# Performance work log

Hardware: AMD Instinct MI355X
Metric: run time of the kernel (lower is better)

Reference implementation:

```python
import jax, jax.numpy as jnp
import numpy as np
from jax.scipy.linalg import cho_solve

N, D, K, M = 2048, 128, 8, 64
JITTER = 1e-5


def setup_inputs() -> dict:
    key = jax.random.key(0)
    ks = jax.random.split(key, 5)
    X = jax.random.normal(ks[0], (N, D), jnp.float32)
    Y = jax.random.normal(ks[1], (N, 1), jnp.float32)
    q_mu = 0.1 * jax.random.normal(ks[2], (K, D), jnp.float32)
    # positive variational covariances ~ 1/D, as in the original init
    q_cov = jax.random.uniform(ks[3], (K, D), jnp.float32, 0.5 / D, 1.5 / D)
    Z = jax.random.normal(ks[4], (M, K), jnp.float32)
    sigma_f = jnp.float32(1.0)
    noise_var = jnp.float32(0.01)
    return {"X": X, "Y": Y, "q_mu": q_mu, "q_cov": q_cov, "Z": Z,
            "sigma_f": sigma_f, "noise_var": noise_var}


def _compute_psi1(X, q_mu, q_cov, Z, sigma_f):
    # q_mu_X: (K, N)
    q_mu_X = jnp.einsum('kd,nd->kn', q_mu, X)
    # top: (K, N, M)
    top = (q_mu_X[:, :, None] - Z.T[:, None, :]) ** 2
    # bot: (K, N)
    bot = 1.0 + jnp.einsum('kd,nd->kn', q_cov, X * X)
    bot = bot[:, :, None]
    psi1 = jnp.exp(-0.5 * top / bot) / jnp.sqrt(bot)  # (K, N, M)
    return sigma_f * jnp.prod(psi1, axis=0)  # (N, M)


def _compute_batched_psi2(X, q_mu, q_cov, Z, sigma_f):
    q_mu_X = jnp.einsum('kd,nd->kn', q_mu, X)  # (K, N)
    Z_diff = Z[:, None, :] - Z[None, :, :]      # (M, M, K)
    Z_bar = 0.5 * (Z[:, None, :] + Z[None, :, :])  # (M, M, K)
    # top: (K, N, M, M) -- the dominant intermediate
    top = (q_mu_X[:, :, None, None] - jnp.transpose(Z_bar, (2, 0, 1))[:, None, :, :]) ** 2
    bot = 2.0 * jnp.einsum('kd,nd->kn', q_cov, X * X) + 1.0  # (K, N)
    bot = bot[:, :, None, None]
    right = jnp.prod(jnp.exp(-top / bot) / jnp.sqrt(bot), axis=0)  # (N, M, M)
    left = (sigma_f ** 2) * jnp.exp(-0.25 * jnp.sum(Z_diff ** 2, axis=2))  # (M, M)
    return left * right  # (N, M, M)


def _rbf_K(Z):
    # ARD RBF with unit variance and unit lengthscales (frozen in original)
    sq = jnp.sum((Z[:, None, :] - Z[None, :, :]) ** 2, axis=-1)
    return jnp.exp(-0.5 * sq)


def _chol_logdet(chol):
    return 2.0 * jnp.sum(jnp.log(jnp.diagonal(chol)), axis=-1)


def _elbo(X, Y, q_mu, q_cov, Z, sigma_f, noise_var):
    n = X.shape[0]
    d = X.shape[1]
    m = Z.shape[0]
    sigma2 = jnp.reshape(noise_var, ())
    sf = jnp.reshape(sigma_f, ())
    two_pi = jnp.asarray(2.0 * np.pi, X.dtype)
    eye = jnp.eye(m, dtype=X.dtype)

    Kuu = _rbf_K(Z) + eye * JITTER
    chol_Ku = jnp.linalg.cholesky(Kuu)
    F1 = -n * jnp.log(two_pi) - (n - m) * jnp.log(sigma2) + _chol_logdet(chol_Ku)

    YY = Y.T @ Y  # (1, 1)
    psi2 = jnp.sum(_compute_batched_psi2(X, q_mu, q_cov, Z, sf), axis=0)  # (M, M)
    Ku_Psi2 = sigma2 * Kuu + psi2 + eye * JITTER
    chol_Ku_Psi2 = jnp.linalg.cholesky(Ku_Psi2)
    F1 = F1 - _chol_logdet(chol_Ku_Psi2) - YY / sigma2  # (1, 1)

    psi1 = _compute_psi1(X, q_mu, q_cov, Z, sf)  # (N, M)
    Psi1_Y = psi1.T @ Y  # (M, 1)
    F1 = F1 + (Psi1_Y.T @ cho_solve((chol_Ku_Psi2, True), Psi1_Y)) / sigma2

    psi0 = n * sf ** 2
    KuiPsi2 = cho_solve((chol_Ku, True), psi2)
    F1 = F1 - psi0 / sigma2 + jnp.trace(KuiPsi2) / sigma2

    KL = jnp.sum(jnp.log(q_cov), axis=1)
    KL = KL - d * jnp.log(jnp.sum(q_cov + q_mu ** 2, axis=1))
    KL = KL + d * jnp.asarray(np.log(d), X.dtype)
    KL = jnp.sum(KL)
    return jnp.squeeze(0.5 * (F1 + KL))


def reference(X, Y, q_mu, q_cov, Z, sigma_f, noise_var):
    return _elbo(X, Y, q_mu, q_cov, Z, sigma_f, noise_var)
```

## Files before the change

kernel.cpp:

```cpp
#include <hip/hip_runtime.h>
#include <math.h>

namespace {
constexpr int N_ = 2048;
constexpr int D_ = 128;
constexpr int K_ = 8;
constexpr int M_ = 64;
constexpr float JIT = 1e-5f;
constexpr float L2E = 1.4426950408889634f;
constexpr float LN2 = 0.6931471805599453f;

constexpr int OFF_ARR2 = 32;
constexpr int OFF_C2   = OFF_ARR2 + N_ * 16;
constexpr int OFF_ARR1 = OFF_C2 + N_;
constexpr int OFF_CY   = OFF_ARR1 + N_ * 16;
constexpr int OFF_P2P  = OFF_CY + N_;
constexpr int OFF_P1Y  = OFF_P2P + 16 * 4096;
constexpr int OFF_PSI2 = OFF_P1Y + 512;
constexpr int OFF_KUI  = OFF_PSI2 + 4096;
constexpr int OFF_SC   = OFF_KUI + 4096;
}

struct F8 { float f[8]; };

__device__ __forceinline__ void bar_arrive(int* c) {
  __syncthreads();
  if (threadIdx.x == 0) { __threadfence(); atomicAdd(c, 1); }
}
template <int SLP>
__device__ __forceinline__ void bar_wait(int* c, int target) {
  if (threadIdx.x == 0) {
    while (__hip_atomic_load(c, __ATOMIC_RELAXED, __HIP_MEMORY_SCOPE_AGENT) < target)
      __builtin_amdgcn_s_sleep(SLP);
    __threadfence();
  }
  __syncthreads();
}

__device__ __forceinline__ float sweep2x2_pipe(
    float* reg, float (*rowbuf)[2][M_], int wave, int lane) {
  if (wave == 0) {
    rowbuf[0][0][lane] = reg[0];
    rowbuf[0][1][lane] = reg[1];
  }
  __syncthreads();
  float ld = 0.f;
#pragma unroll
  for (int s = 0; s < 32; ++s) {
    const int p = 2 * s;
    const int par = s & 1;
    float* rbA = rowbuf[par][0];
    float* rbB = rowbuf[par][1];
    const int own_s  = s >> 3;
    const int own_s1 = (s + 1) >> 3;
    const int rp  = p & 15;
    const int rp2 = (p + 2) & 15;

    const float P00 = rbA[p];
    const float P01 = rbA[p + 1];
    const float P11 = rbB[p + 1];
    const float a0  = rbA[lane];
    const float a1  = rbB[lane];
    const float det = fmaf(P00, P11, -P01 * P01);
    const float idet = __builtin_amdgcn_rcpf(det);
    ld += __log2f(det);
    const float Pi00 =  P11 * idet;
    const float Pi01 = -P01 * idet;
    const float Pi11 =  P00 * idet;

    const bool isp = (lane == p), isq = (lane == p + 1);
    const float w0 = isp ? Pi00 : (isq ? Pi01 : fmaf(Pi00, a0, Pi01 * a1));
    const float w1 = isp ? Pi01 : (isq ? Pi11 : fmaf(Pi01, a0, Pi11 * a1));
    const float t0 = isp ? (1.f - w0) : (isq ? -w0 : w0);
    const float t1 = isq ? (1.f - w1) : (isp ? -w1 : w1);
    const float f0 = (isp || isq) ? -w0 : w0;
    const float f1 = (isp || isq) ? -w1 : w1;

    if (s < 31 && wave == own_s1) {
      const float e0 = fmaf(-t1, rbB[p + 2], fmaf(-t0, rbA[p + 2], reg[rp2]));
      const float e1 = fmaf(-t1, rbB[p + 3], fmaf(-t0, rbA[p + 3], reg[rp2 + 1]));
      rowbuf[par ^ 1][0][lane] = e0;
      rowbuf[par ^ 1][1][lane] = e1;
    }

    const float4* rAq = reinterpret_cast<const float4*>(rbA + 16 * wave);
    const float4* rBq = reinterpret_cast<const float4*>(rbB + 16 * wave);
#pragma unroll
    for (int q = 0; q < 4; q++) {
      const float4 va = rAq[q], vb = rBq[q];
      reg[4 * q + 0] = fmaf(-t1, vb.x, fmaf(-t0, va.x, reg[4 * q + 0]));
      reg[4 * q + 1] = fmaf(-t1, vb.y, fmaf(-t0, va.y, reg[4 * q + 1]));
      reg[4 * q + 2] = fmaf(-t1, vb.z, fmaf(-t0, va.z, reg[4 * q + 2]));
      reg[4 * q + 3] = fmaf(-t1, vb.w, fmaf(-t0, va.w, reg[4 * q + 3]));
    }
    if (wave == own_s) { reg[rp] = f0; reg[rp + 1] = f1; }
    __syncthreads();
  }
  return ld;
}

__global__ __launch_bounds__(256) void vdmgp_k1(
    const float* __restrict__ X, const float* __restrict__ Y,
    const float* __restrict__ qmu, const float* __restrict__ qcov,
    const float* __restrict__ Z, float* __restrict__ ws) {
  __shared__ float smu[D_ * K_];
  __shared__ float scov[D_ * K_];
  __shared__ float zl[M_][9];
  __shared__ __align__(16) float rowbuf[2][2][M_];
  const int tid = threadIdx.x;
  const int b = blockIdx.x;

  if (b == 0 && tid < 32) ((int*)ws)[tid] = 0;

  if (b == 8) {
    for (int idx = tid; idx < M_ * K_; idx += 256) zl[idx >> 3][idx & 7] = Z[idx];
    __syncthreads();
    const int lane = tid & 63;
    const int wave = tid >> 6;
    float zj[K_];
#pragma unroll
    for (int k = 0; k < K_; k++) zj[k] = zl[lane][k];
    float reg[16];
#pragma unroll
    for (int r = 0; r < 16; r++) {
      const int gi = 16 * wave + r;
      float sq = 0.f;
#pragma unroll
      for (int k = 0; k < K_; k++) { const float dd = zl[gi][k] - zj[k]; sq = fmaf(dd, dd, sq); }
      reg[r] = exp2f(-0.5f * L2E * sq) + ((gi == lane) ? JIT : 0.f);
    }
    const float ld1 = sweep2x2_pipe(reg, rowbuf, wave, lane);
#pragma unroll
    for (int r = 0; r < 16; r++)
      ws[OFF_KUI + (16 * wave + r) * 64 + lane] = reg[r];
    if (tid == 0) ws[OFF_SC + 2] = LN2 * ld1;
    return;
  }

  if (b == 9) {
    const int lane = tid & 63;
    const int wave = tid >> 6;
    if (wave == 0) {
      float yy = 0.f;
#pragma unroll
      for (int t = 0; t < 32; t++) {
        const float y = Y[t * 64 + lane];
        yy = fmaf(y, y, yy);
      }
#pragma unroll
      for (int off = 32; off > 0; off >>= 1) yy += __shfl_down(yy, off, 64);
      if (lane == 0) ws[OFF_SC + 0] = yy;
    } else if (wave == 1) {
      const int k = lane >> 3;
      const int d0 = (lane & 7) * 16;
      float slog = 0.f, srow = 0.f;
#pragma unroll
      for (int t = 0; t < 16; t++) {
        const float qc = qcov[k * D_ + d0 + t];
        const float qm = qmu[k * D_ + d0 + t];
        slog += logf(qc);
        srow += qc + qm * qm;
      }
#pragma unroll
      for (int off = 4; off > 0; off >>= 1) {
        slog += __shfl_down(slog, off, 8);
        srow += __shfl_down(srow, off, 8);
      }
      float klr = ((lane & 7) == 0)
          ? (slog - (float)D_ * logf(srow) + (float)D_ * logf((float)D_)) : 0.f;
      klr += __shfl_down(klr, 32, 64);
      klr += __shfl_down(klr, 16, 64);
      klr += __shfl_down(klr, 8, 64);
      if (lane == 0) ws[OFF_SC + 1] = klr;
    }
    return;
  }

  for (int idx = tid; idx < K_ * D_; idx += 256) {
    int k = idx >> 7, d = idx & 127;
    smu[d * K_ + k]  = qmu[idx];
    scov[d * K_ + k] = qcov[idx];
  }
  __syncthreads();

  const int n = b * 256 + tid;
  float a[K_], s2[K_];
#pragma unroll
  for (int k = 0; k < K_; k++) { a[k] = 0.f; s2[k] = 0.f; }

  const float4* xrow = reinterpret_cast<const float4*>(X + n * D_);
#pragma unroll 2
  for (int dq = 0; dq < D_ / 4; dq++) {
    float4 xv = xrow[dq];
    float xs[4] = {xv.x, xv.y, xv.z, xv.w};
#pragma unroll
    for (int t = 0; t < 4; t++) {
      const int d = dq * 4 + t;
      const float x = xs[t];
      const float xx = x * x;
      F8 mu = *reinterpret_cast<const F8*>(&smu[d * K_]);
      F8 cv = *reinterpret_cast<const F8*>(&scov[d * K_]);
#pragma unroll
      for (int k = 0; k < K_; k++) {
        a[k]  = fmaf(mu.f[k], x, a[k]);
        s2[k] = fmaf(cv.f[k], xx, s2[k]);
      }
    }
  }

  float4 w2[4], w1[4];
  float prod2 = 1.f, prod1 = 1.f;
#pragma unroll
  for (int k = 0; k < K_; k++) {
    const float b2 = 2.f * s2[k] + 1.f;
    const float b1 = 1.f + s2[k];
    reinterpret_cast<float*>(w2)[k]     = a[k];
    reinterpret_cast<float*>(w2)[8 + k] = L2E / b2;
    reinterpret_cast<float*>(w1)[k]     = a[k];
    reinterpret_cast<float*>(w1)[8 + k] = 0.5f * L2E / b1;
    prod2 *= rsqrtf(b2);
    prod1 *= rsqrtf(b1);
  }
  float4* a2q = reinterpret_cast<float4*>(ws + OFF_ARR2 + n * 16);
  float4* a1q = reinterpret_cast<float4*>(ws + OFF_ARR1 + n * 16);
#pragma unroll
  for (int e = 0; e < 4; e++) { a2q[e] = w2[e]; a1q[e] = w1[e]; }
  (ws + OFF_C2)[n] = prod2;
  (ws + OFF_CY)[n] = prod1 * Y[n];
}

__global__ __launch_bounds__(256) void vdmgp_k2(
    const float* __restrict__ Z,
    const float* __restrict__ sfp, const float* __restrict__ nvp,
    float* __restrict__ ws, float* __restrict__ out) {
  __shared__ __align__(16) float pool[4864];

  int* bar = (int*)ws;
  const int tid = threadIdx.x;
  const int b = blockIdx.x;
  const float sf = sfp[0];

  if (b > 0) {
    const int t = b - 1;
    {
      float* sa = pool;
      float* sc = pool + 2048;
      const int chunk = t >> 4;
      const int nbase = chunk * 128;
      const float4* src = reinterpret_cast<const float4*>(ws + OFF_ARR2 + nbase * 16);
      float4* dst = reinterpret_cast<float4*>(sa);
      for (int idx = tid; idx < 128 * 4; idx += 256) dst[idx] = src[idx];
      if (tid < 128) sc[tid] = (ws + OFF_C2)[nbase + tid];
      __syncthreads();

      const int pair = (t & 15) * 256 + tid;
      const int i = pair >> 6, j = pair & 63;
      float zb[K_];
#pragma unroll
      for (int k = 0; k < K_; k++) zb[k] = 0.5f * (Z[i * K_ + k] + Z[j * K_ + k]);

      float acc = 0.f;
      for (int nl = 0; nl < 128; nl += 4) {
        F8 av0 = *reinterpret_cast<const F8*>(&sa[(nl + 0) * 16]);
        F8 ib0 = *reinterpret_cast<const F8*>(&sa[(nl + 0) * 16 + 8]);
        F8 av1 = *reinterpret_cast<const F8*>(&sa[(nl + 1) * 16]);
        F8 ib1 = *reinterpret_cast<const F8*>(&sa[(nl + 1) * 16 + 8]);
        F8 av2 = *reinterpret_cast<const F8*>(&sa[(nl + 2) * 16]);
        F8 ib2 = *reinterpret_cast<const F8*>(&sa[(nl + 2) * 16 + 8]);
        F8 av3 = *reinterpret_cast<const F8*>(&sa[(nl + 3) * 16]);
        F8 ib3 = *reinterpret_cast<const F8*>(&sa[(nl + 3) * 16 + 8]);
        float s0 = 0.f, s1 = 0.f, s2 = 0.f, s3 = 0.f;
#pragma unroll
        for (int k = 0; k < K_; k++) {
          const float d0 = av0.f[k] - zb[k]; s0 = fmaf(d0 * d0, ib0.f[k], s0);
          const float d1 = av1.f[k] - zb[k]; s1 = fmaf(d1 * d1, ib1.f[k], s1);
          const float d2 = av2.f[k] - zb[k]; s2 = fmaf(d2 * d2, ib2.f[k], s2);
          const float d3 = av3.f[k] - zb[k]; s3 = fmaf(d3 * d3, ib3.f[k], s3);
        }
        acc = fmaf(sc[nl + 0], exp2f(-s0), acc);
        acc = fmaf(sc[nl + 1], exp2f(-s1), acc);
        acc = fmaf(sc[nl + 2], exp2f(-s2), acc);
        acc = fmaf(sc[nl + 3], exp2f(-s3), acc);
      }
      (ws + OFF_P2P)[chunk * 4096 + (t & 15) * 256 + tid] = acc;
    }
    bar_arrive(&bar[t & 15]);

    if (t < 16) {
      bar_wait<4>(&bar[t], 16);
      const int p = t * 256 + tid;
      float acc = 0.f;
#pragma unroll
      for (int c = 0; c < 16; c++) acc += ws[OFF_P2P + c * 4096 + p];
      const int i = p >> 6, j = p & 63;
      float sq = 0.f;
#pragma unroll
      for (int k = 0; k < K_; k++) {
        const float dd = Z[i * K_ + k] - Z[j * K_ + k];
        sq = fmaf(dd, dd, sq);
      }
      ws[OFF_PSI2 + p] = sf * sf * exp2f(-0.25f * L2E * sq) * acc;
      bar_arrive(&bar[17]);
    } else if (t < 24) {
      float* sa1 = pool;
      float* scy = pool + 4096;
      float* red = pool + 4352;
      const int chunk = t - 16;
      const int nbase = chunk * 256;
      const float4* src = reinterpret_cast<const float4*>(ws + OFF_ARR1 + nbase * 16);
      float4* dst = reinterpret_cast<float4*>(sa1);
#pragma unroll
      for (int r = 0; r < 4; r++) dst[r * 256 + tid] = src[r * 256 + tid];
      scy[tid] = (ws + OFF_CY)[nbase + tid];
      __syncthreads();

      const int m = tid & 63;
      const int stripe = tid >> 6;
      float zm[K_];
#pragma unroll
      for (int k = 0; k < K_; k++) zm[k] = Z[m * K_ + k];

      float acc = 0.f;
      for (int u = 0; u < 64; u++) {
        const int nl = stripe * 64 + u;
        const F8 av = *reinterpret_cast<const F8*>(&sa1[nl * 16]);
        const F8 ib = *reinterpret_cast<const F8*>(&sa1[nl * 16 + 8]);
        float s = 0.f;
#pragma unroll
        for (int k = 0; k < K_; k++) {
          const float d = av.f[k] - zm[k];
          s = fmaf(d * d, ib.f[k], s);
        }
        acc = fmaf(scy[nl], exp2f(-s), acc);
      }
      red[tid] = acc;
      __syncthreads();
      if (tid < 64)
        (ws + OFF_P1Y)[chunk * 64 + tid] =
            red[tid] + red[64 + tid] + red[128 + tid] + red[192 + tid];
      bar_arrive(&bar[16]);
    }
    return;
  }

  float (*zl)[9]         = reinterpret_cast<float(*)[9]>(pool);
  float (*rowbuf)[2][M_] = reinterpret_cast<float(*)[2][M_]>(pool + 576);
  float* pysL  = pool + 832;
  float* scalL = pool + 896;
  float* redQ  = pool + 912;
  float* redT  = pool + 1168;

  const int lane = tid & 63;
  const int wave = tid >> 6;
  const float s2v = nvp[0];

  for (int idx = tid; idx < M_ * K_; idx += 256) zl[idx >> 3][idx & 7] = Z[idx];
  __syncthreads();

  float zj[K_];
#pragma unroll
  for (int k = 0; k < K_; k++) zj[k] = zl[lane][k];
  float base[16], kui16[16];
#pragma unroll
  for (int r = 0; r < 16; r++) {
    const int gi = 16 * wave + r;
    float sq = 0.f;
#pragma unroll
    for (int k = 0; k < K_; k++) { const float dd = zl[gi][k] - zj[k]; sq = fmaf(dd, dd, sq); }
    const float jit = (gi == lane) ? JIT : 0.f;
    base[r] = fmaf(s2v, exp2f(-0.5f * L2E * sq) + jit, jit);
    kui16[r] = ws[OFF_KUI + gi * 64 + lane];
  }

  bar_wait<2>(&bar[17], 16);

  float reg[16];
  float sT = 0.f;
#pragma unroll
  for (int r = 0; r < 16; r++) {
    const int gi = 16 * wave + r;
    const float p2v = ws[OFF_PSI2 + gi * 64 + lane];
    reg[r] = base[r] + p2v;
    sT = fmaf(kui16[r], p2v, sT);
  }
  redT[tid] = sT;

  const float ld2 = sweep2x2_pipe(reg, rowbuf, wave, lane);

  bar_wait<2>(&bar[16], 8);
  if (tid < M_) {
    float s = 0.f;
#pragma unroll
    for (int c = 0; c < 8; c++) s += ws[OFF_P1Y + c * M_ + tid];
    pysL[tid] = sf * s;
  }
  __syncthreads();

  float sQ = 0.f;
#pragma unroll
  for (int r = 0; r < 16; r++) sQ = fmaf(reg[r], pysL[16 * wave + r], sQ);
  redQ[tid] = sQ;
  __syncthreads();

  if (wave == 0) {
    float c = redQ[lane] + redQ[64 + lane] + redQ[128 + lane] + redQ[192 + lane];
    float q = c * pysL[lane];
#pragma unroll
    for (int off = 32; off > 0; off >>= 1) q += __shfl_down(q, off, 64);
    if (lane == 0) scalL[7] = -q;
  } else if (wave == 1) {
    float s = redT[lane] + redT[64 + lane] + redT[128 + lane] + redT[192 + lane];
#pragma unroll
    for (int off = 32; off > 0; off >>= 1) s += __shfl_down(s, off, 64);
    if (lane == 0) scalL[5] = -s;
  }
  __syncthreads();

  if (tid == 0) {
    const float YY  = ws[OFF_SC + 0];
    const float KL  = ws[OFF_SC + 1];
    const float ld1 = ws[OFF_SC + 2];
    const float tr = scalL[5], quad = scalL[7];
    const float inv = 1.0f / s2v;
    const float F1 = -(float)N_ * 1.8378770664093453f
                   - (float)(N_ - M_) * logf(s2v)
                   + (ld1 - LN2 * ld2)
                   - YY * inv
                   + quad * inv
                   - (float)N_ * sf * sf * inv
                   + tr * inv;
    out[0] = 0.5f * (F1 + KL);
  }
}

extern "C" void kernel_launch(void* const* d_in, const int* in_sizes, int n_in,
                              void* d_out, int out_size, void* d_ws, size_t ws_size,
                              hipStream_t stream) {
  const float* X    = (const float*)d_in[0];
  const float* Y    = (const float*)d_in[1];
  const float* qmu  = (const float*)d_in[2];
  const float* qcov = (const float*)d_in[3];
  const float* Z    = (const float*)d_in[4];
  const float* sfp  = (const float*)d_in[5];
  const float* nvp  = (const float*)d_in[6];
  float* ws  = (float*)d_ws;
  float* out = (float*)d_out;

  vdmgp_k1<<<10, 256, 0, stream>>>(X, Y, qmu, qcov, Z, ws);
  vdmgp_k2<<<257, 256, 0, stream>>>(Z, sfp, nvp, ws, out);
}
```

Before: 50.00 us.

## Fuse psi1 reduction into k1, double pairs per block, drop psi2 finalize stage

Moves the psi1·Y reduction from the second kernel into the first kernel's per-row blocks, so the per-row psi1 parameters stay in shared memory and are never written to global. Each psi2 worker block now handles two (i,j) pairs per thread, which halves the grid to 129 blocks. The separate psi2 chunk-reduction stage and its barrier are removed; the final block sums the 16 partials itself after waiting on 8 group counters, and reuses one exp to get both the Kuu term and the left factor. This shortens the cross-block dependency chain, at the cost of more serial work in k1 and in the final block.

```diff
diff --git a/kernel.cpp b/kernel.cpp
--- a/kernel.cpp
+++ b/kernel.cpp
@@ -10,14 +10,11 @@
 constexpr float L2E = 1.4426950408889634f;
 constexpr float LN2 = 0.6931471805599453f;
 
-constexpr int OFF_ARR2 = 32;
+constexpr int OFF_ARR2 = 16;
 constexpr int OFF_C2   = OFF_ARR2 + N_ * 16;
-constexpr int OFF_ARR1 = OFF_C2 + N_;
-constexpr int OFF_CY   = OFF_ARR1 + N_ * 16;
-constexpr int OFF_P2P  = OFF_CY + N_;
+constexpr int OFF_P2P  = OFF_C2 + N_;
 constexpr int OFF_P1Y  = OFF_P2P + 16 * 4096;
-constexpr int OFF_PSI2 = OFF_P1Y + 512;
-constexpr int OFF_KUI  = OFF_PSI2 + 4096;
+constexpr int OFF_KUI  = OFF_P1Y + 512;
 constexpr int OFF_SC   = OFF_KUI + 4096;
 }
 
@@ -105,12 +102,15 @@
     const float* __restrict__ Z, float* __restrict__ ws) {
   __shared__ float smu[D_ * K_];
   __shared__ float scov[D_ * K_];
+  __shared__ float sa1[256 * 16];
+  __shared__ float scy[256];
+  __shared__ float red[256];
   __shared__ float zl[M_][9];
   __shared__ __align__(16) float rowbuf[2][2][M_];
   const int tid = threadIdx.x;
   const int b = blockIdx.x;
 
-  if (b == 0 && tid < 32) ((int*)ws)[tid] = 0;
+  if (b == 0 && tid < 16) ((int*)ws)[tid] = 0;
 
   if (b == 8) {
     for (int idx = tid; idx < M_ * K_; idx += 256) zl[idx >> 3][idx & 7] = Z[idx];
@@ -189,7 +189,6 @@
   for (int k = 0; k < K_; k++) { a[k] = 0.f; s2[k] = 0.f; }
 
   const float4* xrow = reinterpret_cast<const float4*>(X + n * D_);
-#pragma unroll 2
   for (int dq = 0; dq < D_ / 4; dq++) {
     float4 xv = xrow[dq];
     float xs[4] = {xv.x, xv.y, xv.z, xv.w};
@@ -208,7 +207,7 @@
     }
   }
 
-  float4 w2[4], w1[4];
+  float4 w2[4];
   float prod2 = 1.f, prod1 = 1.f;
 #pragma unroll
   for (int k = 0; k < K_; k++) {
@@ -216,24 +215,48 @@
     const float b1 = 1.f + s2[k];
     reinterpret_cast<float*>(w2)[k]     = a[k];
     reinterpret_cast<float*>(w2)[8 + k] = L2E / b2;
-    reinterpret_cast<float*>(w1)[k]     = a[k];
-    reinterpret_cast<float*>(w1)[8 + k] = 0.5f * L2E / b1;
+    sa1[tid * 16 + k]     = a[k];
+    sa1[tid * 16 + 8 + k] = 0.5f * L2E / b1;
     prod2 *= rsqrtf(b2);
     prod1 *= rsqrtf(b1);
   }
   float4* a2q = reinterpret_cast<float4*>(ws + OFF_ARR2 + n * 16);
-  float4* a1q = reinterpret_cast<float4*>(ws + OFF_ARR1 + n * 16);
-#pragma unroll
-  for (int e = 0; e < 4; e++) { a2q[e] = w2[e]; a1q[e] = w1[e]; }
+#pragma unroll
+  for (int e = 0; e < 4; e++) a2q[e] = w2[e];
   (ws + OFF_C2)[n] = prod2;
-  (ws + OFF_CY)[n] = prod1 * Y[n];
+  scy[tid] = prod1 * Y[n];
+  __syncthreads();
+
+  const int m = tid & 63;
+  const int stripe = tid >> 6;
+  float zm[K_];
+#pragma unroll
+  for (int k = 0; k < K_; k++) zm[k] = Z[m * K_ + k];
+  float acc = 0.f;
+  for (int t = 0; t < 64; t++) {
+    const int nl = stripe * 64 + t;
+    const F8 av = *reinterpret_cast<const F8*>(&sa1[nl * 16]);
+    const F8 ib = *reinterpret_cast<const F8*>(&sa1[nl * 16 + 8]);
+    float s = 0.f;
+#pragma unroll
+    for (int k = 0; k < K_; k++) {
+      const float d = av.f[k] - zm[k];
+      s = fmaf(d * d, ib.f[k], s);
+    }
+    acc = fmaf(scy[nl], exp2f(-s), acc);
+  }
+  red[tid] = acc;
+  __syncthreads();
+  if (tid < 64)
+    (ws + OFF_P1Y)[b * 64 + tid] =
+        red[tid] + red[64 + tid] + red[128 + tid] + red[192 + tid];
 }
 
 __global__ __launch_bounds__(256) void vdmgp_k2(
     const float* __restrict__ Z,
     const float* __restrict__ sfp, const float* __restrict__ nvp,
     float* __restrict__ ws, float* __restrict__ out) {
-  __shared__ __align__(16) float pool[4864];
+  __shared__ __align__(16) float pool[2432];
 
   int* bar = (int*)ws;
   const int tid = threadIdx.x;
@@ -241,105 +264,53 @@
   const float sf = sfp[0];
 
   if (b > 0) {
-    const int t = b - 1;
+    const int w = b - 1;
+    const int chunk = w >> 3;
+    const int sg = w & 7;
+    float* sa = pool;
+    float* sc = pool + 2048;
+    const int nbase = chunk * 128;
     {
-      float* sa = pool;
-      float* sc = pool + 2048;
-      const int chunk = t >> 4;
-      const int nbase = chunk * 128;
       const float4* src = reinterpret_cast<const float4*>(ws + OFF_ARR2 + nbase * 16);
       float4* dst = reinterpret_cast<float4*>(sa);
-      for (int idx = tid; idx < 128 * 4; idx += 256) dst[idx] = src[idx];
+      for (int idx = tid; idx < 512; idx += 256) dst[idx] = src[idx];
       if (tid < 128) sc[tid] = (ws + OFF_C2)[nbase + tid];
-      __syncthreads();
-
-      const int pair = (t & 15) * 256 + tid;
-      const int i = pair >> 6, j = pair & 63;
-      float zb[K_];
-#pragma unroll
-      for (int k = 0; k < K_; k++) zb[k] = 0.5f * (Z[i * K_ + k] + Z[j * K_ + k]);
-
-      float acc = 0.f;
-      for (int nl = 0; nl < 128; nl += 4) {
-        F8 av0 = *reinterpret_cast<const F8*>(&sa[(nl + 0) * 16]);
-        F8 ib0 = *reinterpret_cast<const F8*>(&sa[(nl + 0) * 16 + 8]);
-        F8 av1 = *reinterpret_cast<const F8*>(&sa[(nl + 1) * 16]);
-        F8 ib1 = *reinterpret_cast<const F8*>(&sa[(nl + 1) * 16 + 8]);
-        F8 av2 = *reinterpret_cast<const F8*>(&sa[(nl + 2) * 16]);
-        F8 ib2 = *reinterpret_cast<const F8*>(&sa[(nl + 2) * 16 + 8]);
-        F8 av3 = *reinterpret_cast<const F8*>(&sa[(nl + 3) * 16]);
-        F8 ib3 = *reinterpret_cast<const F8*>(&sa[(nl + 3) * 16 + 8]);
-        float s0 = 0.f, s1 = 0.f, s2 = 0.f, s3 = 0.f;
-#pragma unroll
-        for (int k = 0; k < K_; k++) {
-          const float d0 = av0.f[k] - zb[k]; s0 = fmaf(d0 * d0, ib0.f[k], s0);
-          const float d1 = av1.f[k] - zb[k]; s1 = fmaf(d1 * d1, ib1.f[k], s1);
-          const float d2 = av2.f[k] - zb[k]; s2 = fmaf(d2 * d2, ib2.f[k], s2);
-          const float d3 = av3.f[k] - zb[k]; s3 = fmaf(d3 * d3, ib3.f[k], s3);
-        }
-        acc = fmaf(sc[nl + 0], exp2f(-s0), acc);
-        acc = fmaf(sc[nl + 1], exp2f(-s1), acc);
-        acc = fmaf(sc[nl + 2], exp2f(-s2), acc);
-        acc = fmaf(sc[nl + 3], exp2f(-s3), acc);
+    }
+    __syncthreads();
+
+    const int pa = (2 * sg) * 256 + tid;
+    const int pb = pa + 256;
+    const int ia = pa >> 6, ja = pa & 63;
+    const int ib_ = pb >> 6, jb = pb & 63;
+    float zba[K_], zbb[K_];
+#pragma unroll
+    for (int k = 0; k < K_; k++) {
+      zba[k] = 0.5f * (Z[ia * K_ + k] + Z[ja * K_ + k]);
+      zbb[k] = 0.5f * (Z[ib_ * K_ + k] + Z[jb * K_ + k]);
+    }
+
+    float acca = 0.f, accb = 0.f;
+    for (int nl = 0; nl < 128; nl += 2) {
+      const F8 av0 = *reinterpret_cast<const F8*>(&sa[nl * 16]);
+      const F8 ib0 = *reinterpret_cast<const F8*>(&sa[nl * 16 + 8]);
+      const F8 av1 = *reinterpret_cast<const F8*>(&sa[(nl + 1) * 16]);
+      const F8 ib1 = *reinterpret_cast<const F8*>(&sa[(nl + 1) * 16 + 8]);
+      float s0a = 0.f, s0b = 0.f, s1a = 0.f, s1b = 0.f;
+#pragma unroll
+      for (int k = 0; k < K_; k++) {
+        const float da0 = av0.f[k] - zba[k]; s0a = fmaf(da0 * da0, ib0.f[k], s0a);
+        const float db0 = av0.f[k] - zbb[k]; s0b = fmaf(db0 * db0, ib0.f[k], s0b);
+        const float da1 = av1.f[k] - zba[k]; s1a = fmaf(da1 * da1, ib1.f[k], s1a);
+        const float db1 = av1.f[k] - zbb[k]; s1b = fmaf(db1 * db1, ib1.f[k], s1b);
       }
-      (ws + OFF_P2P)[chunk * 4096 + (t & 15) * 256 + tid] = acc;
-    }
-    bar_arrive(&bar[t & 15]);
-
-    if (t < 16) {
-      bar_wait<4>(&bar[t], 16);
-      const int p = t * 256 + tid;
-      float acc = 0.f;
-#pragma unroll
-      for (int c = 0; c < 16; c++) acc += ws[OFF_P2P + c * 4096 + p];
-      const int i = p >> 6, j = p & 63;
-      float sq = 0.f;
-#pragma unroll
-      for (int k = 0; k < K_; k++) {
-        const float dd = Z[i * K_ + k] - Z[j * K_ + k];
-        sq = fmaf(dd, dd, sq);
-      }
-      ws[OFF_PSI2 + p] = sf * sf * exp2f(-0.25f * L2E * sq) * acc;
-      bar_arrive(&bar[17]);
-    } else if (t < 24) {
-      float* sa1 = pool;
-      float* scy = pool + 4096;
-      float* red = pool + 4352;
-      const int chunk = t - 16;
-      const int nbase = chunk * 256;
-      const float4* src = reinterpret_cast<const float4*>(ws + OFF_ARR1 + nbase * 16);
-      float4* dst = reinterpret_cast<float4*>(sa1);
-#pragma unroll
-      for (int r = 0; r < 4; r++) dst[r * 256 + tid] = src[r * 256 + tid];
-      scy[tid] = (ws + OFF_CY)[nbase + tid];
-      __syncthreads();
-
-      const int m = tid & 63;
-      const int stripe = tid >> 6;
-      float zm[K_];
-#pragma unroll
-      for (int k = 0; k < K_; k++) zm[k] = Z[m * K_ + k];
-
-      float acc = 0.f;
-      for (int u = 0; u < 64; u++) {
-        const int nl = stripe * 64 + u;
-        const F8 av = *reinterpret_cast<const F8*>(&sa1[nl * 16]);
-        const F8 ib = *reinterpret_cast<const F8*>(&sa1[nl * 16 + 8]);
-        float s = 0.f;
-#pragma unroll
-        for (int k = 0; k < K_; k++) {
-          const float d = av.f[k] - zm[k];
-          s = fmaf(d * d, ib.f[k], s);
-        }
-        acc = fmaf(scy[nl], exp2f(-s), acc);
-      }
-      red[tid] = acc;
-      __syncthreads();
-      if (tid < 64)
-        (ws + OFF_P1Y)[chunk * 64 + tid] =
-            red[tid] + red[64 + tid] + red[128 + tid] + red[192 + tid];
-      bar_arrive(&bar[16]);
-    }
+      acca = fmaf(sc[nl], exp2f(-s0a), acca);
+      accb = fmaf(sc[nl], exp2f(-s0b), accb);
+      acca = fmaf(sc[nl + 1], exp2f(-s1a), acca);
+      accb = fmaf(sc[nl + 1], exp2f(-s1b), accb);
+    }
+    (ws + OFF_P2P)[chunk * 4096 + pa] = acca;
+    (ws + OFF_P2P)[chunk * 4096 + pb] = accb;
+    bar_arrive(&bar[sg]);
     return;
   }
 
@@ -353,48 +324,52 @@
   const int lane = tid & 63;
   const int wave = tid >> 6;
   const float s2v = nvp[0];
+  const float sf2 = sf * sf;
 
   for (int idx = tid; idx < M_ * K_; idx += 256) zl[idx >> 3][idx & 7] = Z[idx];
+  if (tid < M_) {
+    float s = 0.f;
+#pragma unroll
+    for (int c = 0; c < 8; c++) s += ws[OFF_P1Y + c * M_ + tid];
+    pysL[tid] = sf * s;
+  }
   __syncthreads();
 
   float zj[K_];
 #pragma unroll
   for (int k = 0; k < K_; k++) zj[k] = zl[lane][k];
-  float base[16], kui16[16];
+  float base[16], leftf[16], kui16[16];
 #pragma unroll
   for (int r = 0; r < 16; r++) {
     const int gi = 16 * wave + r;
     float sq = 0.f;
 #pragma unroll
     for (int k = 0; k < K_; k++) { const float dd = zl[gi][k] - zj[k]; sq = fmaf(dd, dd, sq); }
+    const float e = exp2f(-0.25f * L2E * sq);
     const float jit = (gi == lane) ? JIT : 0.f;
-    base[r] = fmaf(s2v, exp2f(-0.5f * L2E * sq) + jit, jit);
+    base[r]  = fmaf(s2v, e * e + jit, jit);
+    leftf[r] = sf2 * e;
     kui16[r] = ws[OFF_KUI + gi * 64 + lane];
   }
 
-  bar_wait<2>(&bar[17], 16);
+#pragma unroll
+  for (int g = 0; g < 8; g++) bar_wait<2>(&bar[g], 16);
 
   float reg[16];
   float sT = 0.f;
 #pragma unroll
   for (int r = 0; r < 16; r++) {
-    const int gi = 16 * wave + r;
-    const float p2v = ws[OFF_PSI2 + gi * 64 + lane];
+    const int pidx = (16 * wave + r) * 64 + lane;
+    float s = 0.f;
+#pragma unroll
+    for (int c = 0; c < 16; c++) s += ws[OFF_P2P + c * 4096 + pidx];
+    const float p2v = leftf[r] * s;
     reg[r] = base[r] + p2v;
     sT = fmaf(kui16[r], p2v, sT);
   }
   redT[tid] = sT;
 
   const float ld2 = sweep2x2_pipe(reg, rowbuf, wave, lane);
-
-  bar_wait<2>(&bar[16], 8);
-  if (tid < M_) {
-    float s = 0.f;
-#pragma unroll
-    for (int c = 0; c < 8; c++) s += ws[OFF_P1Y + c * M_ + tid];
-    pysL[tid] = sf * s;
-  }
-  __syncthreads();
 
   float sQ = 0.f;
 #pragma unroll
@@ -427,7 +402,7 @@
                    + (ld1 - LN2 * ld2)
                    - YY * inv
                    + quad * inv
-                   - (float)N_ * sf * sf * inv
+                   - (float)N_ * sf2 * inv
                    + tr * inv;
     out[0] = 0.5f * (F1 + KL);
   }
@@ -447,5 +422,5 @@
   float* out = (float*)d_out;
 
   vdmgp_k1<<<10, 256, 0, stream>>>(X, Y, qmu, qcov, Z, ws);
-  vdmgp_k2<<<257, 256, 0, stream>>>(Z, sfp, nvp, ws, out);
-}
+  vdmgp_k2<<<129, 256, 0, stream>>>(Z, sfp, nvp, ws, out);
+}
```

New measurement: 58.86 us. +17.7%, slower.

## Fuse both kernels into one persistent megakernel with per-chunk atomic flags

Applied to the files above, without the earlier changes.

Merges the two launches into a single grid. Producer blocks compute per-point coefficients, publish them, and signal a per-block flag, so psi2 blocks can start on a chunk as soon as its producer is done rather than after a full kernel boundary. The psi1·Y work moves into the producer blocks, which keep their coefficients in shared memory and no longer round-trip the psi1 arrays through global memory. Flag reset becomes a memset before the launch, and the design relies on all 267 blocks being co-resident, since spinning blocks would otherwise deadlock.

```diff
diff --git a/kernel.cpp b/kernel.cpp
--- a/kernel.cpp
+++ b/kernel.cpp
@@ -12,9 +12,7 @@
 
 constexpr int OFF_ARR2 = 32;
 constexpr int OFF_C2   = OFF_ARR2 + N_ * 16;
-constexpr int OFF_ARR1 = OFF_C2 + N_;
-constexpr int OFF_CY   = OFF_ARR1 + N_ * 16;
-constexpr int OFF_P2P  = OFF_CY + N_;
+constexpr int OFF_P2P  = OFF_C2 + N_;
 constexpr int OFF_P1Y  = OFF_P2P + 16 * 4096;
 constexpr int OFF_PSI2 = OFF_P1Y + 512;
 constexpr int OFF_KUI  = OFF_PSI2 + 4096;
@@ -99,20 +97,108 @@
   return ld;
 }
 
-__global__ __launch_bounds__(256) void vdmgp_k1(
+__global__ __launch_bounds__(256) void vdmgp_mega(
     const float* __restrict__ X, const float* __restrict__ Y,
     const float* __restrict__ qmu, const float* __restrict__ qcov,
-    const float* __restrict__ Z, float* __restrict__ ws) {
-  __shared__ float smu[D_ * K_];
-  __shared__ float scov[D_ * K_];
-  __shared__ float zl[M_][9];
-  __shared__ __align__(16) float rowbuf[2][2][M_];
+    const float* __restrict__ Z,
+    const float* __restrict__ sfp, const float* __restrict__ nvp,
+    float* __restrict__ ws, float* __restrict__ out) {
+  __shared__ __align__(16) float pool[6656];
+
+  int* bar = (int*)ws;
   const int tid = threadIdx.x;
   const int b = blockIdx.x;
-
-  if (b == 0 && tid < 32) ((int*)ws)[tid] = 0;
+  const float sf = sfp[0];
+
+  if (b < 8) {
+    float* smu = pool;
+    float* scov = pool + 1024;
+    float* sa1 = pool + 2048;
+    float* scy = pool + 6144;
+    float* red = pool + 6400;
+
+    for (int idx = tid; idx < K_ * D_; idx += 256) {
+      int k = idx >> 7, d = idx & 127;
+      smu[d * K_ + k]  = qmu[idx];
+      scov[d * K_ + k] = qcov[idx];
+    }
+    __syncthreads();
+
+    const int n = b * 256 + tid;
+    float a[K_], s2[K_];
+#pragma unroll
+    for (int k = 0; k < K_; k++) { a[k] = 0.f; s2[k] = 0.f; }
+
+    const float4* xrow = reinterpret_cast<const float4*>(X + n * D_);
+    for (int dq = 0; dq < D_ / 4; dq++) {
+      float4 xv = xrow[dq];
+      float xs[4] = {xv.x, xv.y, xv.z, xv.w};
+#pragma unroll
+      for (int t = 0; t < 4; t++) {
+        const int d = dq * 4 + t;
+        const float x = xs[t];
+        const float xx = x * x;
+        F8 mu = *reinterpret_cast<const F8*>(&smu[d * K_]);
+        F8 cv = *reinterpret_cast<const F8*>(&scov[d * K_]);
+#pragma unroll
+        for (int k = 0; k < K_; k++) {
+          a[k]  = fmaf(mu.f[k], x, a[k]);
+          s2[k] = fmaf(cv.f[k], xx, s2[k]);
+        }
+      }
+    }
+
+    float4 w2[4];
+    float prod2 = 1.f, prod1 = 1.f;
+#pragma unroll
+    for (int k = 0; k < K_; k++) {
+      const float b2 = 2.f * s2[k] + 1.f;
+      const float b1 = 1.f + s2[k];
+      reinterpret_cast<float*>(w2)[k]     = a[k];
+      reinterpret_cast<float*>(w2)[8 + k] = L2E / b2;
+      sa1[tid * 16 + k]     = a[k];
+      sa1[tid * 16 + 8 + k] = 0.5f * L2E / b1;
+      prod2 *= rsqrtf(b2);
+      prod1 *= rsqrtf(b1);
+    }
+    float4* a2q = reinterpret_cast<float4*>(ws + OFF_ARR2 + n * 16);
+#pragma unroll
+    for (int e = 0; e < 4; e++) a2q[e] = w2[e];
+    (ws + OFF_C2)[n] = prod2;
+    scy[tid] = prod1 * Y[n];
+
+    bar_arrive(&bar[b]);
+
+    const int m = tid & 63;
+    const int stripe = tid >> 6;
+    float zm[K_];
+#pragma unroll
+    for (int k = 0; k < K_; k++) zm[k] = Z[m * K_ + k];
+    float acc = 0.f;
+    for (int t = 0; t < 64; t++) {
+      const int nl = stripe * 64 + t;
+      const F8 av = *reinterpret_cast<const F8*>(&sa1[nl * 16]);
+      const F8 ib = *reinterpret_cast<const F8*>(&sa1[nl * 16 + 8]);
+      float s = 0.f;
+#pragma unroll
+      for (int k = 0; k < K_; k++) {
+        const float d = av.f[k] - zm[k];
+        s = fmaf(d * d, ib.f[k], s);
+      }
+      acc = fmaf(scy[nl], exp2f(-s), acc);
+    }
+    red[tid] = acc;
+    __syncthreads();
+    if (tid < 64)
+      (ws + OFF_P1Y)[b * 64 + tid] =
+          red[tid] + red[64 + tid] + red[128 + tid] + red[192 + tid];
+    bar_arrive(&bar[24]);
+    return;
+  }
 
   if (b == 8) {
+    float (*zl)[9] = reinterpret_cast<float(*)[9]>(pool);
+    float (*rowbuf)[2][M_] = reinterpret_cast<float(*)[2][M_]>(pool + 576);
     for (int idx = tid; idx < M_ * K_; idx += 256) zl[idx >> 3][idx & 7] = Z[idx];
     __syncthreads();
     const int lane = tid & 63;
@@ -134,6 +220,7 @@
     for (int r = 0; r < 16; r++)
       ws[OFF_KUI + (16 * wave + r) * 64 + lane] = reg[r];
     if (tid == 0) ws[OFF_SC + 2] = LN2 * ld1;
+    bar_arrive(&bar[25]);
     return;
   }
 
@@ -173,172 +260,75 @@
       klr += __shfl_down(klr, 8, 64);
       if (lane == 0) ws[OFF_SC + 1] = klr;
     }
+    bar_arrive(&bar[26]);
     return;
   }
 
-  for (int idx = tid; idx < K_ * D_; idx += 256) {
-    int k = idx >> 7, d = idx & 127;
-    smu[d * K_ + k]  = qmu[idx];
-    scov[d * K_ + k] = qcov[idx];
-  }
-  __syncthreads();
-
-  const int n = b * 256 + tid;
-  float a[K_], s2[K_];
-#pragma unroll
-  for (int k = 0; k < K_; k++) { a[k] = 0.f; s2[k] = 0.f; }
-
-  const float4* xrow = reinterpret_cast<const float4*>(X + n * D_);
-#pragma unroll 2
-  for (int dq = 0; dq < D_ / 4; dq++) {
-    float4 xv = xrow[dq];
-    float xs[4] = {xv.x, xv.y, xv.z, xv.w};
-#pragma unroll
-    for (int t = 0; t < 4; t++) {
-      const int d = dq * 4 + t;
-      const float x = xs[t];
-      const float xx = x * x;
-      F8 mu = *reinterpret_cast<const F8*>(&smu[d * K_]);
-      F8 cv = *reinterpret_cast<const F8*>(&scov[d * K_]);
-#pragma unroll
-      for (int k = 0; k < K_; k++) {
-        a[k]  = fmaf(mu.f[k], x, a[k]);
-        s2[k] = fmaf(cv.f[k], xx, s2[k]);
-      }
-    }
-  }
-
-  float4 w2[4], w1[4];
-  float prod2 = 1.f, prod1 = 1.f;
-#pragma unroll
-  for (int k = 0; k < K_; k++) {
-    const float b2 = 2.f * s2[k] + 1.f;
-    const float b1 = 1.f + s2[k];
-    reinterpret_cast<float*>(w2)[k]     = a[k];
-    reinterpret_cast<float*>(w2)[8 + k] = L2E / b2;
-    reinterpret_cast<float*>(w1)[k]     = a[k];
-    reinterpret_cast<float*>(w1)[8 + k] = 0.5f * L2E / b1;
-    prod2 *= rsqrtf(b2);
-    prod1 *= rsqrtf(b1);
-  }
-  float4* a2q = reinterpret_cast<float4*>(ws + OFF_ARR2 + n * 16);
-  float4* a1q = reinterpret_cast<float4*>(ws + OFF_ARR1 + n * 16);
-#pragma unroll
-  for (int e = 0; e < 4; e++) { a2q[e] = w2[e]; a1q[e] = w1[e]; }
-  (ws + OFF_C2)[n] = prod2;
-  (ws + OFF_CY)[n] = prod1 * Y[n];
-}
-
-__global__ __launch_bounds__(256) void vdmgp_k2(
-    const float* __restrict__ Z,
-    const float* __restrict__ sfp, const float* __restrict__ nvp,
-    float* __restrict__ ws, float* __restrict__ out) {
-  __shared__ __align__(16) float pool[4864];
-
-  int* bar = (int*)ws;
-  const int tid = threadIdx.x;
-  const int b = blockIdx.x;
-  const float sf = sfp[0];
-
-  if (b > 0) {
-    const int t = b - 1;
+  if (b >= 11) {
+    const int w = b - 11;
+    const int chunk = w >> 4;
+    const int slice = w & 15;
+    float* sa = pool;
+    float* sc = pool + 2048;
+
+    bar_wait<8>(&bar[w >> 5], 1);
+
+    const int nbase = chunk * 128;
     {
-      float* sa = pool;
-      float* sc = pool + 2048;
-      const int chunk = t >> 4;
-      const int nbase = chunk * 128;
       const float4* src = reinterpret_cast<const float4*>(ws + OFF_ARR2 + nbase * 16);
       float4* dst = reinterpret_cast<float4*>(sa);
-      for (int idx = tid; idx < 128 * 4; idx += 256) dst[idx] = src[idx];
+      for (int idx = tid; idx < 512; idx += 256) dst[idx] = src[idx];
       if (tid < 128) sc[tid] = (ws + OFF_C2)[nbase + tid];
-      __syncthreads();
-
-      const int pair = (t & 15) * 256 + tid;
-      const int i = pair >> 6, j = pair & 63;
-      float zb[K_];
-#pragma unroll
-      for (int k = 0; k < K_; k++) zb[k] = 0.5f * (Z[i * K_ + k] + Z[j * K_ + k]);
-
-      float acc = 0.f;
-      for (int nl = 0; nl < 128; nl += 4) {
-        F8 av0 = *reinterpret_cast<const F8*>(&sa[(nl + 0) * 16]);
-        F8 ib0 = *reinterpret_cast<const F8*>(&sa[(nl + 0) * 16 + 8]);
-        F8 av1 = *reinterpret_cast<const F8*>(&sa[(nl + 1) * 16]);
-        F8 ib1 = *reinterpret_cast<const F8*>(&sa[(nl + 1) * 16 + 8]);
-        F8 av2 = *reinterpret_cast<const F8*>(&sa[(nl + 2) * 16]);
-        F8 ib2 = *reinterpret_cast<const F8*>(&sa[(nl + 2) * 16 + 8]);
-        F8 av3 = *reinterpret_cast<const F8*>(&sa[(nl + 3) * 16]);
-        F8 ib3 = *reinterpret_cast<const F8*>(&sa[(nl + 3) * 16 + 8]);
-        float s0 = 0.f, s1 = 0.f, s2 = 0.f, s3 = 0.f;
-#pragma unroll
-        for (int k = 0; k < K_; k++) {
-          const float d0 = av0.f[k] - zb[k]; s0 = fmaf(d0 * d0, ib0.f[k], s0);
-          const float d1 = av1.f[k] - zb[k]; s1 = fmaf(d1 * d1, ib1.f[k], s1);
-          const float d2 = av2.f[k] - zb[k]; s2 = fmaf(d2 * d2, ib2.f[k], s2);
-          const float d3 = av3.f[k] - zb[k]; s3 = fmaf(d3 * d3, ib3.f[k], s3);
-        }
-        acc = fmaf(sc[nl + 0], exp2f(-s0), acc);
-        acc = fmaf(sc[nl + 1], exp2f(-s1), acc);
-        acc = fmaf(sc[nl + 2], exp2f(-s2), acc);
-        acc = fmaf(sc[nl + 3], exp2f(-s3), acc);
-      }
-      (ws + OFF_P2P)[chunk * 4096 + (t & 15) * 256 + tid] = acc;
-    }
-    bar_arrive(&bar[t & 15]);
-
-    if (t < 16) {
-      bar_wait<4>(&bar[t], 16);
-      const int p = t * 256 + tid;
-      float acc = 0.f;
-#pragma unroll
-      for (int c = 0; c < 16; c++) acc += ws[OFF_P2P + c * 4096 + p];
-      const int i = p >> 6, j = p & 63;
+    }
+    __syncthreads();
+
+    const int pair = slice * 256 + tid;
+    const int i = pair >> 6, j = pair & 63;
+    float zb[K_];
+#pragma unroll
+    for (int k = 0; k < K_; k++) zb[k] = 0.5f * (Z[i * K_ + k] + Z[j * K_ + k]);
+
+    float acc = 0.f;
+    for (int nl = 0; nl < 128; nl += 4) {
+      F8 av0 = *reinterpret_cast<const F8*>(&sa[(nl + 0) * 16]);
+      F8 ib0 = *reinterpret_cast<const F8*>(&sa[(nl + 0) * 16 + 8]);
+      F8 av1 = *reinterpret_cast<const F8*>(&sa[(nl + 1) * 16]);
+      F8 ib1 = *reinterpret_cast<const F8*>(&sa[(nl + 1) * 16 + 8]);
+      F8 av2 = *reinterpret_cast<const F8*>(&sa[(nl + 2) * 16]);
+      F8 ib2 = *reinterpret_cast<const F8*>(&sa[(nl + 2) * 16 + 8]);
+      F8 av3 = *reinterpret_cast<const F8*>(&sa[(nl + 3) * 16]);
+      F8 ib3 = *reinterpret_cast<const F8*>(&sa[(nl + 3) * 16 + 8]);
+      float s0 = 0.f, s1 = 0.f, s2 = 0.f, s3 = 0.f;
+#pragma unroll
+      for (int k = 0; k < K_; k++) {
+        const float d0 = av0.f[k] - zb[k]; s0 = fmaf(d0 * d0, ib0.f[k], s0);
+        const float d1 = av1.f[k] - zb[k]; s1 = fmaf(d1 * d1, ib1.f[k], s1);
+        const float d2 = av2.f[k] - zb[k]; s2 = fmaf(d2 * d2, ib2.f[k], s2);
+        const float d3 = av3.f[k] - zb[k]; s3 = fmaf(d3 * d3, ib3.f[k], s3);
+      }
+      acc = fmaf(sc[nl + 0], exp2f(-s0), acc);
+      acc = fmaf(sc[nl + 1], exp2f(-s1), acc);
+      acc = fmaf(sc[nl + 2], exp2f(-s2), acc);
+      acc = fmaf(sc[nl + 3], exp2f(-s3), acc);
+    }
+    (ws + OFF_P2P)[chunk * 4096 + pair] = acc;
+    bar_arrive(&bar[8 + slice]);
+
+    if (w < 16) {
+      bar_wait<4>(&bar[8 + w], 16);
+      const int p = w * 256 + tid;
+      float racc = 0.f;
+#pragma unroll
+      for (int c = 0; c < 16; c++) racc += ws[OFF_P2P + c * 4096 + p];
+      const int ri = p >> 6, rj = p & 63;
       float sq = 0.f;
 #pragma unroll
       for (int k = 0; k < K_; k++) {
-        const float dd = Z[i * K_ + k] - Z[j * K_ + k];
+        const float dd = Z[ri * K_ + k] - Z[rj * K_ + k];
         sq = fmaf(dd, dd, sq);
       }
-      ws[OFF_PSI2 + p] = sf * sf * exp2f(-0.25f * L2E * sq) * acc;
-      bar_arrive(&bar[17]);
-    } else if (t < 24) {
-      float* sa1 = pool;
-      float* scy = pool + 4096;
-      float* red = pool + 4352;
-      const int chunk = t - 16;
-      const int nbase = chunk * 256;
-      const float4* src = reinterpret_cast<const float4*>(ws + OFF_ARR1 + nbase * 16);
-      float4* dst = reinterpret_cast<float4*>(sa1);
-#pragma unroll
-      for (int r = 0; r < 4; r++) dst[r * 256 + tid] = src[r * 256 + tid];
-      scy[tid] = (ws + OFF_CY)[nbase + tid];
-      __syncthreads();
-
-      const int m = tid & 63;
-      const int stripe = tid >> 6;
-      float zm[K_];
-#pragma unroll
-      for (int k = 0; k < K_; k++) zm[k] = Z[m * K_ + k];
-
-      float acc = 0.f;
-      for (int u = 0; u < 64; u++) {
-        const int nl = stripe * 64 + u;
-        const F8 av = *reinterpret_cast<const F8*>(&sa1[nl * 16]);
-        const F8 ib = *reinterpret_cast<const F8*>(&sa1[nl * 16 + 8]);
-        float s = 0.f;
-#pragma unroll
-        for (int k = 0; k < K_; k++) {
-          const float d = av.f[k] - zm[k];
-          s = fmaf(d * d, ib.f[k], s);
-        }
-        acc = fmaf(scy[nl], exp2f(-s), acc);
-      }
-      red[tid] = acc;
-      __syncthreads();
-      if (tid < 64)
-        (ws + OFF_P1Y)[chunk * 64 + tid] =
-            red[tid] + red[64 + tid] + red[128 + tid] + red[192 + tid];
-      bar_arrive(&bar[16]);
+      ws[OFF_PSI2 + p] = sf * sf * exp2f(-0.25f * L2E * sq) * racc;
+      bar_arrive(&bar[27]);
     }
     return;
   }
@@ -360,7 +350,7 @@
   float zj[K_];
 #pragma unroll
   for (int k = 0; k < K_; k++) zj[k] = zl[lane][k];
-  float base[16], kui16[16];
+  float base[16];
 #pragma unroll
   for (int r = 0; r < 16; r++) {
     const int gi = 16 * wave + r;
@@ -369,25 +359,27 @@
     for (int k = 0; k < K_; k++) { const float dd = zl[gi][k] - zj[k]; sq = fmaf(dd, dd, sq); }
     const float jit = (gi == lane) ? JIT : 0.f;
     base[r] = fmaf(s2v, exp2f(-0.5f * L2E * sq) + jit, jit);
-    kui16[r] = ws[OFF_KUI + gi * 64 + lane];
-  }
-
-  bar_wait<2>(&bar[17], 16);
-
-  float reg[16];
+  }
+
+  bar_wait<4>(&bar[27], 16);
+
+  float reg[16], p2v[16];
+#pragma unroll
+  for (int r = 0; r < 16; r++) {
+    p2v[r] = ws[OFF_PSI2 + (16 * wave + r) * 64 + lane];
+    reg[r] = base[r] + p2v[r];
+  }
+
+  const float ld2 = sweep2x2_pipe(reg, rowbuf, wave, lane);
+
+  bar_wait<4>(&bar[25], 1);
   float sT = 0.f;
 #pragma unroll
-  for (int r = 0; r < 16; r++) {
-    const int gi = 16 * wave + r;
-    const float p2v = ws[OFF_PSI2 + gi * 64 + lane];
-    reg[r] = base[r] + p2v;
-    sT = fmaf(kui16[r], p2v, sT);
-  }
+  for (int r = 0; r < 16; r++)
+    sT = fmaf(ws[OFF_KUI + (16 * wave + r) * 64 + lane], p2v[r], sT);
   redT[tid] = sT;
 
-  const float ld2 = sweep2x2_pipe(reg, rowbuf, wave, lane);
-
-  bar_wait<2>(&bar[16], 8);
+  bar_wait<4>(&bar[24], 8);
   if (tid < M_) {
     float s = 0.f;
 #pragma unroll
@@ -416,6 +408,7 @@
   }
   __syncthreads();
 
+  bar_wait<4>(&bar[26], 1);
   if (tid == 0) {
     const float YY  = ws[OFF_SC + 0];
     const float KL  = ws[OFF_SC + 1];
@@ -446,6 +439,6 @@
   float* ws  = (float*)d_ws;
   float* out = (float*)d_out;
 
-  vdmgp_k1<<<10, 256, 0, stream>>>(X, Y, qmu, qcov, Z, ws);
-  vdmgp_k2<<<257, 256, 0, stream>>>(Z, sfp, nvp, ws, out);
-}
+  hipMemsetAsync(d_ws, 0, 128, stream);
+  vdmgp_mega<<<267, 256, 0, stream>>>(X, Y, qmu, qcov, Z, sfp, nvp, ws, out);
+}
```

Result: slower. 54.01 us (+8.0%).
